# Optimization experiments

Measured on AMD Instinct MI355X. Metric: run time of the kernel, lower is better.

Reference implementation:

```python
import jax, jax.numpy as jnp
import numpy as np

VOCAB = 2048
CHORD_VOCAB = 60
SCALE_W = 0.1
REP_W = 0.05
CHORD_W = 0.2
WINDOW = 8  # repetition look-back window


def setup_inputs() -> dict:
    key = jax.random.key(0)
    ks = jax.random.split(key, 7)
    B, S = 4, 2048
    return {
        "logits": jax.random.normal(ks[0], (B, S, VOCAB), dtype=jnp.float32),
        "chord_logits": jax.random.normal(ks[1], (B, S, CHORD_VOCAB), dtype=jnp.float32),
        "scale_logits": jax.random.normal(ks[2], (B, S, 12), dtype=jnp.float32),
        "scale_targets": jax.random.uniform(ks[3], (B, S, 12), dtype=jnp.float32),
        "target_ids": jax.random.randint(ks[4], (B, S), 0, VOCAB, dtype=jnp.int64),
        "key_ids": jax.random.randint(ks[5], (B,), 0, 12, dtype=jnp.int64),
        "chord_targets": jax.random.randint(ks[6], (B, S), 0, CHORD_VOCAB, dtype=jnp.int64),
    }


def _ce_ignore(logits, targets, ignore_index=-100):
    # cross entropy with ignore_index, mean over valid tokens
    logp = jax.nn.log_softmax(logits, axis=-1)
    valid = (targets != ignore_index)
    safe = jnp.where(valid, targets, 0)
    nll = -jnp.take_along_axis(logp, safe[..., None], axis=-1)[..., 0]
    denom = jnp.maximum(valid.sum(), 1)
    return jnp.sum(nll * valid) / denom.astype(logits.dtype)


def _repetition_loss(target_ids, dtype):
    # input_ids = [0, target_ids[:, :-1]] (teacher-forced inputs)
    B, S = target_ids.shape
    input_ids = jnp.concatenate(
        [jnp.zeros((B, 1), dtype=target_ids.dtype), target_ids[:, :-1]], axis=1)
    # sliding-window histogram: counts[b,pos,v] = #{t in [max(0,pos-8), pos) : ids[b,t]==v}
    oh = jax.nn.one_hot(input_ids, VOCAB, dtype=dtype)          # [B,S,V]
    cs = jnp.cumsum(oh, axis=1)                                  # cs[p] = sum_{0..p}
    a = jnp.pad(cs, ((0, 0), (1, 0), (0, 0)))[:, :S]             # cs[pos-1]
    b = jnp.pad(cs, ((0, 0), (WINDOW + 1, 0), (0, 0)))[:, :S]    # cs[pos-9]
    counts = a - b                                               # zero at pos=0 automatically
    # penalty = -0.5*counts; rep_loss = -penalty.mean() = 0.5*mean(counts)
    return 0.5 * jnp.mean(counts)


def _bce_with_logits(x, z):
    # numerically stable mean BCE-with-logits
    return jnp.mean(jnp.maximum(x, 0) - x * z + jnp.log1p(jnp.exp(-jnp.abs(x))))


def reference(logits, chord_logits, scale_logits, scale_targets,
              target_ids, key_ids, chord_targets):
    main_loss = _ce_ignore(logits, target_ids)
    rep_loss = _repetition_loss(target_ids, logits.dtype)
    chord_loss = _ce_ignore(chord_logits, chord_targets, ignore_index=-(10**9))  # no ignores present
    scale_loss = _bce_with_logits(scale_logits, scale_targets)
    total = main_loss + REP_W * rep_loss + CHORD_W * chord_loss + SCALE_W * scale_loss
    return total
```

## Files before the change

kernel.cpp:

```cpp
#include <hip/hip_runtime.h>
#include <math.h>


#define VOCAB 2048
#define CHORDV 60

__device__ __forceinline__ float waveRedMax(float v) {
#pragma unroll
    for (int off = 32; off > 0; off >>= 1)
        v = fmaxf(v, __shfl_xor(v, off, 64));
    return v;
}

__device__ __forceinline__ float waveRedSum(float v) {
#pragma unroll
    for (int off = 32; off > 0; off >>= 1)
        v += __shfl_xor(v, off, 64);
    return v;
}

__global__ __launch_bounds__(256) void ce_main_kernel(
    const float* __restrict__ logits, const int* __restrict__ tgt,
    float* __restrict__ nll_out, float* __restrict__ valid_out) {
    const int row = blockIdx.x;
    const int tid = threadIdx.x;
    const int lane = tid & 63;
    const int wave = tid >> 6;
    const float* p = logits + (size_t)row * VOCAB;

    float4 a = ((const float4*)p)[tid];
    float4 b = ((const float4*)p)[tid + 256];

    float m = fmaxf(fmaxf(fmaxf(a.x, a.y), fmaxf(a.z, a.w)),
                    fmaxf(fmaxf(b.x, b.y), fmaxf(b.z, b.w)));

    __shared__ float red[4];
    float wm = waveRedMax(m);
    if (lane == 0) red[wave] = wm;
    __syncthreads();
    const float bm = fmaxf(fmaxf(red[0], red[1]), fmaxf(red[2], red[3]));
    __syncthreads();

    float s = expf(a.x - bm) + expf(a.y - bm) + expf(a.z - bm) + expf(a.w - bm)
            + expf(b.x - bm) + expf(b.y - bm) + expf(b.z - bm) + expf(b.w - bm);
    float ws_ = waveRedSum(s);
    if (lane == 0) red[wave] = ws_;
    __syncthreads();

    if (tid == 0) {
        const float bs = red[0] + red[1] + red[2] + red[3];
        const int t = tgt[row];
        float nll = 0.0f, valid = 0.0f;
        if (t != -100) {
            const float xt = p[t];
            nll = -(xt - bm - logf(bs));
            valid = 1.0f;
        }
        nll_out[row] = nll;
        valid_out[row] = valid;
    }
}

__global__ __launch_bounds__(256) void ce_chord_kernel(
    const float* __restrict__ cl, const int* __restrict__ ct,
    float* __restrict__ nll_out, float* __restrict__ valid_out, int nrows) {
    const int lane = threadIdx.x & 63;
    const int row = blockIdx.x * 4 + (threadIdx.x >> 6);
    if (row >= nrows) return;
    const float* p = cl + (size_t)row * CHORDV;

    float x = (lane < CHORDV) ? p[lane] : -INFINITY;
    float m = waveRedMax(x);
    float e = (lane < CHORDV) ? expf(x - m) : 0.0f;
    float s = waveRedSum(e);

    if (lane == 0) {
        const int t = ct[row];
        float nll = 0.0f, valid = 0.0f;
        if (t != -1000000000) {
            nll = -(p[t] - m - logf(s));
            valid = 1.0f;
        }
        nll_out[row] = nll;
        valid_out[row] = valid;
    }
}

__device__ __forceinline__ float bce1(float x, float z) {
    return fmaxf(x, 0.0f) - x * z + log1pf(expf(-fabsf(x)));
}

__global__ __launch_bounds__(256) void bce_scale_kernel(
    const float* __restrict__ x, const float* __restrict__ z,
    float* __restrict__ partials, int n4) {
    const int i = blockIdx.x * 256 + threadIdx.x;
    const int lane = threadIdx.x & 63;
    const int wave = threadIdx.x >> 6;
    float s = 0.0f;
    if (i < n4) {
        float4 xv = ((const float4*)x)[i];
        float4 zv = ((const float4*)z)[i];
        s = bce1(xv.x, zv.x) + bce1(xv.y, zv.y) + bce1(xv.z, zv.z) + bce1(xv.w, zv.w);
    }
    __shared__ float red[4];
    float wsum = waveRedSum(s);
    if (lane == 0) red[wave] = wsum;
    __syncthreads();
    if (threadIdx.x == 0)
        partials[blockIdx.x] = red[0] + red[1] + red[2] + red[3];
}

__device__ __forceinline__ float blockSum256(float v, float* red) {
    const int lane = threadIdx.x & 63;
    const int wave = threadIdx.x >> 6;
    float w = waveRedSum(v);
    __syncthreads();
    if (lane == 0) red[wave] = w;
    __syncthreads();
    return red[0] + red[1] + red[2] + red[3];
}

__global__ __launch_bounds__(256) void finalize_kernel(
    const float* __restrict__ ws, int BS, int S, int nScaleBlocks, int scaleN,
    float* __restrict__ out) {
    const int tid = threadIdx.x;
    float sm = 0.f, svm = 0.f, sc = 0.f, svc = 0.f, ss = 0.f;
    for (int i = tid; i < BS; i += 256) {
        sm  += ws[i];
        svm += ws[BS + i];
        sc  += ws[2 * BS + i];
        svc += ws[3 * BS + i];
    }
    for (int i = tid; i < nScaleBlocks; i += 256) ss += ws[4 * BS + i];

    __shared__ float red[4];
    sm  = blockSum256(sm,  red);
    svm = blockSum256(svm, red);
    sc  = blockSum256(sc,  red);
    svc = blockSum256(svc, red);
    ss  = blockSum256(ss,  red);

    if (tid == 0) {
        const float main_loss  = sm / fmaxf(svm, 1.0f);
        const float chord_loss = sc / fmaxf(svc, 1.0f);
        const float scale_loss = ss / (float)scaleN;
        double wsum = (S >= 8) ? (28.0 + 8.0 * (double)(S - 8))
                               : ((double)S * (double)(S - 1) * 0.5);
        const float rep_loss = (float)(0.5 * wsum / ((double)S * (double)VOCAB));
        out[0] = main_loss + 0.05f * rep_loss + 0.2f * chord_loss + 0.1f * scale_loss;
    }
}

extern "C" void kernel_launch(void* const* d_in, const int* in_sizes, int n_in,
                              void* d_out, int out_size, void* d_ws, size_t ws_size,
                              hipStream_t stream) {
    const float* logits        = (const float*)d_in[0];
    const float* chord_logits  = (const float*)d_in[1];
    const float* scale_logits  = (const float*)d_in[2];
    const float* scale_targets = (const float*)d_in[3];
    const int*   target_ids    = (const int*)d_in[4];
    const int*   chord_targets = (const int*)d_in[6];

    const int BS = in_sizes[4];
    const int B  = in_sizes[5];
    const int S  = BS / B;
    const int scaleN = in_sizes[2];
    const int n4 = scaleN / 4;
    const int nScaleBlocks = (n4 + 255) / 256;

    float* ws = (float*)d_ws;

    ce_main_kernel<<<BS, 256, 0, stream>>>(logits, target_ids, ws, ws + BS);
    ce_chord_kernel<<<(BS + 3) / 4, 256, 0, stream>>>(chord_logits, chord_targets,
                                                      ws + 2 * BS, ws + 3 * BS, BS);
    bce_scale_kernel<<<nScaleBlocks, 256, 0, stream>>>(scale_logits, scale_targets,
                                                       ws + 4 * BS, n4);
    finalize_kernel<<<1, 256, 0, stream>>>(ws, BS, S, nScaleBlocks, scaleN,
                                           (float*)d_out);
}
```

Baseline: 117.6 us.

## Fuse main CE, chord CE and BCE into one launch with packed partials

Merges the three leaf kernels into one kernel that assigns each block to main CE, chord CE or BCE by its block index, cutting two kernel launches. The target logit is now taken from registers through shared memory instead of a second global read. Nontemporal loads, fast __expf/__logf intrinsics and per-block chord partials packed as float2 are added, and the finalize kernel runs 1024 threads over fewer partials. This trades some accuracy from the fast math and makes the kernel branch more heterogeneous.

```diff
diff --git a/kernel.cpp b/kernel.cpp
--- a/kernel.cpp
+++ b/kernel.cpp
@@ -4,6 +4,8 @@
 
 #define VOCAB 2048
 #define CHORDV 60
+
+typedef float vf4 __attribute__((ext_vector_type(4)));
 
 __device__ __forceinline__ float waveRedMax(float v) {
 #pragma unroll
@@ -19,126 +21,149 @@
     return v;
 }
 
-__global__ __launch_bounds__(256) void ce_main_kernel(
+__device__ __forceinline__ float bce1(float x, float z) {
+    return fmaxf(x, 0.0f) - x * z + __logf(1.0f + __expf(-fabsf(x)));
+}
+
+__global__ __launch_bounds__(256) void fused_leaf_kernel(
     const float* __restrict__ logits, const int* __restrict__ tgt,
-    float* __restrict__ nll_out, float* __restrict__ valid_out) {
-    const int row = blockIdx.x;
+    const float* __restrict__ chordL, const int* __restrict__ chordT,
+    const float* __restrict__ sx, const float* __restrict__ sz,
+    float2* __restrict__ mainNV, float2* __restrict__ chordNV,
+    float* __restrict__ scaleP, int BS, int chordBlocks, int n4) {
+    const int bid = blockIdx.x;
     const int tid = threadIdx.x;
     const int lane = tid & 63;
     const int wave = tid >> 6;
-    const float* p = logits + (size_t)row * VOCAB;
-
-    float4 a = ((const float4*)p)[tid];
-    float4 b = ((const float4*)p)[tid + 256];
-
-    float m = fmaxf(fmaxf(fmaxf(a.x, a.y), fmaxf(a.z, a.w)),
-                    fmaxf(fmaxf(b.x, b.y), fmaxf(b.z, b.w)));
 
     __shared__ float red[4];
-    float wm = waveRedMax(m);
-    if (lane == 0) red[wave] = wm;
-    __syncthreads();
-    const float bm = fmaxf(fmaxf(red[0], red[1]), fmaxf(red[2], red[3]));
-    __syncthreads();
-
-    float s = expf(a.x - bm) + expf(a.y - bm) + expf(a.z - bm) + expf(a.w - bm)
-            + expf(b.x - bm) + expf(b.y - bm) + expf(b.z - bm) + expf(b.w - bm);
-    float ws_ = waveRedSum(s);
-    if (lane == 0) red[wave] = ws_;
-    __syncthreads();
-
-    if (tid == 0) {
-        const float bs = red[0] + red[1] + red[2] + red[3];
+    __shared__ float xt_sh;
+    __shared__ float2 csh[4];
+
+    if (bid < BS) {
+        const int row = bid;
         const int t = tgt[row];
-        float nll = 0.0f, valid = 0.0f;
-        if (t != -100) {
-            const float xt = p[t];
-            nll = -(xt - bm - logf(bs));
-            valid = 1.0f;
-        }
-        nll_out[row] = nll;
-        valid_out[row] = valid;
-    }
-}
-
-__global__ __launch_bounds__(256) void ce_chord_kernel(
-    const float* __restrict__ cl, const int* __restrict__ ct,
-    float* __restrict__ nll_out, float* __restrict__ valid_out, int nrows) {
-    const int lane = threadIdx.x & 63;
-    const int row = blockIdx.x * 4 + (threadIdx.x >> 6);
-    if (row >= nrows) return;
-    const float* p = cl + (size_t)row * CHORDV;
-
-    float x = (lane < CHORDV) ? p[lane] : -INFINITY;
-    float m = waveRedMax(x);
-    float e = (lane < CHORDV) ? expf(x - m) : 0.0f;
-    float s = waveRedSum(e);
-
-    if (lane == 0) {
-        const int t = ct[row];
-        float nll = 0.0f, valid = 0.0f;
-        if (t != -1000000000) {
-            nll = -(p[t] - m - logf(s));
-            valid = 1.0f;
-        }
-        nll_out[row] = nll;
-        valid_out[row] = valid;
-    }
-}
-
-__device__ __forceinline__ float bce1(float x, float z) {
-    return fmaxf(x, 0.0f) - x * z + log1pf(expf(-fabsf(x)));
-}
-
-__global__ __launch_bounds__(256) void bce_scale_kernel(
-    const float* __restrict__ x, const float* __restrict__ z,
-    float* __restrict__ partials, int n4) {
-    const int i = blockIdx.x * 256 + threadIdx.x;
-    const int lane = threadIdx.x & 63;
-    const int wave = threadIdx.x >> 6;
-    float s = 0.0f;
-    if (i < n4) {
-        float4 xv = ((const float4*)x)[i];
-        float4 zv = ((const float4*)z)[i];
-        s = bce1(xv.x, zv.x) + bce1(xv.y, zv.y) + bce1(xv.z, zv.z) + bce1(xv.w, zv.w);
-    }
-    __shared__ float red[4];
-    float wsum = waveRedSum(s);
-    if (lane == 0) red[wave] = wsum;
-    __syncthreads();
-    if (threadIdx.x == 0)
-        partials[blockIdx.x] = red[0] + red[1] + red[2] + red[3];
-}
-
-__device__ __forceinline__ float blockSum256(float v, float* red) {
+        const float* p = logits + (size_t)row * VOCAB;
+
+        vf4 a = __builtin_nontemporal_load(((const vf4*)p) + tid);
+        vf4 b = __builtin_nontemporal_load(((const vf4*)p) + tid + 256);
+
+        const bool valid = (t >= 0) && (t < VOCAB);
+        if (valid) {
+            const int owner = t >> 2;
+            const int comp = t & 3;
+            if (owner == tid) {
+                xt_sh = a[comp];
+            } else if (owner == tid + 256) {
+                xt_sh = b[comp];
+            }
+        }
+
+        float m = fmaxf(fmaxf(fmaxf(a[0], a[1]), fmaxf(a[2], a[3])),
+                        fmaxf(fmaxf(b[0], b[1]), fmaxf(b[2], b[3])));
+        float wm = waveRedMax(m);
+        if (lane == 0) red[wave] = wm;
+        __syncthreads();
+        const float bm = fmaxf(fmaxf(red[0], red[1]), fmaxf(red[2], red[3]));
+        __syncthreads();
+
+        float s = __expf(a[0] - bm) + __expf(a[1] - bm) + __expf(a[2] - bm) + __expf(a[3] - bm)
+                + __expf(b[0] - bm) + __expf(b[1] - bm) + __expf(b[2] - bm) + __expf(b[3] - bm);
+        float ws_ = waveRedSum(s);
+        if (lane == 0) red[wave] = ws_;
+        __syncthreads();
+
+        if (tid == 0) {
+            const float bs = red[0] + red[1] + red[2] + red[3];
+            float2 nv = make_float2(0.0f, 0.0f);
+            if (valid) {
+                nv.x = -(xt_sh - bm - __logf(bs));
+                nv.y = 1.0f;
+            }
+            mainNV[row] = nv;
+        }
+    } else if (bid < BS + chordBlocks) {
+        const int cb = bid - BS;
+        const int row = cb * 4 + wave;
+        float2 nv = make_float2(0.0f, 0.0f);
+        if (row < BS) {
+            const float* p = chordL + (size_t)row * CHORDV;
+            const int t = chordT[row];
+            float x = (lane < CHORDV) ? p[lane] : -INFINITY;
+            float m = waveRedMax(x);
+            float e = (lane < CHORDV) ? __expf(x - m) : 0.0f;
+            float s = waveRedSum(e);
+            if (t != -1000000000) {
+                nv.x = -(p[t] - m - __logf(s));
+                nv.y = 1.0f;
+            }
+        }
+        if (lane == 0) csh[wave] = nv;
+        __syncthreads();
+        if (tid == 0) {
+            chordNV[cb] = make_float2(csh[0].x + csh[1].x + csh[2].x + csh[3].x,
+                                      csh[0].y + csh[1].y + csh[2].y + csh[3].y);
+        }
+    } else {
+        const int sb = bid - BS - chordBlocks;
+        const int i = sb * 256 + tid;
+        float s = 0.0f;
+        if (i < n4) {
+            float4 xv = ((const float4*)sx)[i];
+            float4 zv = ((const float4*)sz)[i];
+            s = bce1(xv.x, zv.x) + bce1(xv.y, zv.y) + bce1(xv.z, zv.z) + bce1(xv.w, zv.w);
+        }
+        float wsum = waveRedSum(s);
+        if (lane == 0) red[wave] = wsum;
+        __syncthreads();
+        if (tid == 0) scaleP[sb] = red[0] + red[1] + red[2] + red[3];
+    }
+}
+
+__device__ __forceinline__ float blockSum1024(float v, float* red16) {
     const int lane = threadIdx.x & 63;
     const int wave = threadIdx.x >> 6;
     float w = waveRedSum(v);
     __syncthreads();
-    if (lane == 0) red[wave] = w;
+    if (lane == 0) red16[wave] = w;
     __syncthreads();
-    return red[0] + red[1] + red[2] + red[3];
-}
-
-__global__ __launch_bounds__(256) void finalize_kernel(
-    const float* __restrict__ ws, int BS, int S, int nScaleBlocks, int scaleN,
-    float* __restrict__ out) {
+    float r = 0.0f;
+#pragma unroll
+    for (int k = 0; k < 16; ++k) r += red16[k];
+    return r;
+}
+
+__global__ __launch_bounds__(1024) void finalize_kernel(
+    const float2* __restrict__ mainNV, const float2* __restrict__ chordNV,
+    const float* __restrict__ scaleP, int BS, int chordBlocks, int nScaleBlocks,
+    int S, int scaleN, float* __restrict__ out) {
     const int tid = threadIdx.x;
     float sm = 0.f, svm = 0.f, sc = 0.f, svc = 0.f, ss = 0.f;
-    for (int i = tid; i < BS; i += 256) {
-        sm  += ws[i];
-        svm += ws[BS + i];
-        sc  += ws[2 * BS + i];
-        svc += ws[3 * BS + i];
-    }
-    for (int i = tid; i < nScaleBlocks; i += 256) ss += ws[4 * BS + i];
-
-    __shared__ float red[4];
-    sm  = blockSum256(sm,  red);
-    svm = blockSum256(svm, red);
-    sc  = blockSum256(sc,  red);
-    svc = blockSum256(svc, red);
-    ss  = blockSum256(ss,  red);
+
+    const float4* m4 = (const float4*)mainNV;
+    for (int i = tid; i < BS / 2; i += 1024) {
+        float4 v = m4[i];
+        sm += v.x + v.z;
+        svm += v.y + v.w;
+    }
+    if ((BS & 1) && tid == 0) { float2 v = mainNV[BS - 1]; sm += v.x; svm += v.y; }
+
+    const float4* c4 = (const float4*)chordNV;
+    for (int i = tid; i < chordBlocks / 2; i += 1024) {
+        float4 v = c4[i];
+        sc += v.x + v.z;
+        svc += v.y + v.w;
+    }
+    if ((chordBlocks & 1) && tid == 0) { float2 v = chordNV[chordBlocks - 1]; sc += v.x; svc += v.y; }
+
+    for (int i = tid; i < nScaleBlocks; i += 1024) ss += scaleP[i];
+
+    __shared__ float red16[16];
+    sm  = blockSum1024(sm,  red16);
+    svm = blockSum1024(svm, red16);
+    sc  = blockSum1024(sc,  red16);
+    svc = blockSum1024(svc, red16);
+    ss  = blockSum1024(ss,  red16);
 
     if (tid == 0) {
         const float main_loss  = sm / fmaxf(svm, 1.0f);
@@ -167,14 +192,18 @@
     const int scaleN = in_sizes[2];
     const int n4 = scaleN / 4;
     const int nScaleBlocks = (n4 + 255) / 256;
-
-    float* ws = (float*)d_ws;
-
-    ce_main_kernel<<<BS, 256, 0, stream>>>(logits, target_ids, ws, ws + BS);
-    ce_chord_kernel<<<(BS + 3) / 4, 256, 0, stream>>>(chord_logits, chord_targets,
-                                                      ws + 2 * BS, ws + 3 * BS, BS);
-    bce_scale_kernel<<<nScaleBlocks, 256, 0, stream>>>(scale_logits, scale_targets,
-                                                       ws + 4 * BS, n4);
-    finalize_kernel<<<1, 256, 0, stream>>>(ws, BS, S, nScaleBlocks, scaleN,
-                                           (float*)d_out);
-}
+    const int chordBlocks = (BS + 3) / 4;
+
+    float2* mainNV  = (float2*)d_ws;
+    float2* chordNV = mainNV + BS;
+    float*  scaleP  = (float*)(chordNV + chordBlocks);
+
+    const int totalBlocks = BS + chordBlocks + nScaleBlocks;
+    fused_leaf_kernel<<<totalBlocks, 256, 0, stream>>>(
+        logits, target_ids, chord_logits, chord_targets,
+        scale_logits, scale_targets, mainNV, chordNV, scaleP,
+        BS, chordBlocks, n4);
+    finalize_kernel<<<1, 1024, 0, stream>>>(mainNV, chordNV, scaleP,
+                                            BS, chordBlocks, nScaleBlocks,
+                                            S, scaleN, (float*)d_out);
+}
```

After: 113.8 us (median of 2 runs). 1.03x faster.
